# Kernel tuning notes

Measured on AMD Instinct MI355X. Metric: run time of the kernel, lower is better.

## Reference

```python
import jax, jax.numpy as jnp
import numpy as np

TWO_PI = 2.0 * np.pi


def setup_inputs() -> dict:
    key = jax.random.key(0)
    ks = jax.random.split(key, 6)
    n1 = n2 = n3 = 20
    nk, ni, nspin = 4, 16, 2
    # Invertible, physically plausible lattice (~8 Bohr cubic cell + jitter)
    A = jnp.eye(3, dtype=jnp.float32) * 8.0 + 0.05 * jax.random.normal(ks[0], (3, 3), jnp.float32)
    k_grid = 0.1 * jax.random.normal(ks[1], (nk, 3), jnp.float32)
    cg_real = jax.random.normal(ks[2], (nspin, nk, ni, n1, n2, n3), jnp.float32)
    cg_imag = jax.random.normal(ks[3], (nspin, nk, ni, n1, n2, n3), jnp.float32)
    # Real-space evaluation grid: fractional coords in [0,1)^3 mapped through A
    frac = jax.random.uniform(ks[4], (n1, n2, n3, 3), jnp.float32)
    r = frac @ A
    return {"A": A, "k_grid": k_grid, "cg_real": cg_real, "cg_imag": cg_imag, "r": r}


def reference(A, k_grid, cg_real, cg_imag, r):
    # cg: [spin, nk, ni, n1, n2, n3] complex plane-wave coefficients
    cg = cg_real + 1j * cg_imag
    n1, n2, n3 = cg.shape[-3:]
    # Integer FFT frequency mesh m -> reciprocal-lattice vectors G = m @ B,
    # B rows are reciprocal basis: B = 2*pi * inv(A)^T  (A rows = lattice vecs)
    f1 = jnp.fft.fftfreq(n1) * n1
    f2 = jnp.fft.fftfreq(n2) * n2
    f3 = jnp.fft.fftfreq(n3) * n3
    m = jnp.stack(jnp.meshgrid(f1, f2, f3, indexing="ij"), axis=-1).astype(A.dtype)  # [n1,n2,n3,3]
    B = TWO_PI * jnp.linalg.inv(A).T
    G = (m @ B).reshape(-1, 3)                      # [nG, 3]
    vol = jnp.abs(jnp.linalg.det(A))
    Rf = r.reshape(-1, 3)                           # [nR, 3]
    # Plane-wave synthesis: psi_{s,k,i}(r) = exp(i k.r)/sqrt(vol) * sum_G c_G exp(i G.r)
    # (equivalent to the triple-nested vmap over the grid dims, fully vectorized)
    phase_g = jnp.exp(1j * (Rf @ G.T))              # [nR, nG] complex
    dens = cg.reshape(*cg.shape[:3], -1)            # [spin, nk, ni, nG]
    psi = jnp.einsum("skin,rn->skir", dens, phase_g)  # [spin, nk, ni, nR]
    phase_k = jnp.exp(1j * (Rf @ k_grid.T))         # [nR, nk]
    psi = psi * jnp.moveaxis(phase_k, 0, -1)[None, :, None, :]
    psi = psi / jnp.sqrt(vol).astype(psi.real.dtype)
    # [spin, nk, ni, n1, n2, n3] -- matches moveaxis(range(3), range(-3,0))
    return psi.reshape(*cg.shape[:3], *r.shape[:-1])
```

## Files before the change

### kernel.cpp

```cpp
#include <hip/hip_runtime.h>

typedef __attribute__((ext_vector_type(4))) float f32x4;
typedef __attribute__((ext_vector_type(8))) short s16x8;

#define NSKIN 128
#define NG    8000
#define NRPT  8000
#define MT    128
#define NT    128
#define KK    32
#define KCH   1000
#define NKC   8
#define NRB   64
#define TPB   512

__device__ __forceinline__ float sin_rev(float u){ float r; asm("v_sin_f32 %0, %1" : "=v"(r) : "v"(u)); return r; }
__device__ __forceinline__ float cos_rev(float u){ float r; asm("v_cos_f32 %0, %1" : "=v"(r) : "v"(u)); return r; }
__device__ __forceinline__ unsigned int cvt_pk(float lo, float hi){
    unsigned int r; asm("v_cvt_pk_bf16_f32 %0, %1, %2" : "=v"(r) : "v"(lo), "v"(hi)); return r;
}
__device__ __forceinline__ s16x8 bneg(s16x8 v){
    int4 u = *(int4*)&v;
    u.x ^= 0x80008000; u.y ^= 0x80008000; u.z ^= 0x80008000; u.w ^= 0x80008000;
    return *(s16x8*)&u;
}
__device__ __forceinline__ int swz(int row, int kg){
    return row*64 + ((kg ^ ((row>>1)&3))<<4);
}

__global__ __launch_bounds__(TPB, 4) void bloch_mfma4(
    const float* __restrict__ Amat, const float* __restrict__ kgrid,
    const float* __restrict__ cgr,  const float* __restrict__ cgi,
    const float* __restrict__ rpts, float* __restrict__ out, int out_size)
{
    __shared__ float fracS[NT][4];
    __shared__ float rkS[NT][4];
    __shared__ unsigned short Ar[MT*KK], Ai[MT*KK];
    __shared__ unsigned short Bc[NT*KK], Bs[NT*KK];
    __shared__ float invAS[9];
    __shared__ float scaleS;

    const int tid = threadIdx.x;
    const int bid = blockIdx.x;
    const int kc  = bid >> 6;
    const int rb  = bid & 63;
    const int r_base  = rb * NT;
    const int k_begin = kc * KCH;
    const int k_end   = k_begin + KCH;

    if (tid == 0) {
        float a00=Amat[0],a01=Amat[1],a02=Amat[2];
        float a10=Amat[3],a11=Amat[4],a12=Amat[5];
        float a20=Amat[6],a21=Amat[7],a22=Amat[8];
        float c00 =  (a11*a22 - a12*a21);
        float c01 = -(a10*a22 - a12*a20);
        float c02 =  (a10*a21 - a11*a20);
        float det = a00*c00 + a01*c01 + a02*c02;
        float id  = 1.0f/det;
        invAS[0] =  c00*id;
        invAS[1] = -(a01*a22 - a02*a21)*id;
        invAS[2] =  (a01*a12 - a02*a11)*id;
        invAS[3] =  c01*id;
        invAS[4] =  (a00*a22 - a02*a20)*id;
        invAS[5] = -(a00*a12 - a02*a10)*id;
        invAS[6] =  c02*id;
        invAS[7] = -(a00*a21 - a01*a20)*id;
        invAS[8] =  (a00*a11 - a01*a10)*id;
        scaleS   = rsqrtf(fabsf(det));
    }
    __syncthreads();

    if (tid < NT) {
        int rg = r_base + tid; if (rg > NRPT-1) rg = NRPT-1;
        float r0 = rpts[rg*3+0], r1 = rpts[rg*3+1], r2 = rpts[rg*3+2];
        fracS[tid][0] = r0*invAS[0] + r1*invAS[3] + r2*invAS[6];
        fracS[tid][1] = r0*invAS[1] + r1*invAS[4] + r2*invAS[7];
        fracS[tid][2] = r0*invAS[2] + r1*invAS[5] + r2*invAS[8];
        #pragma unroll
        for (int kk = 0; kk < 4; ++kk)
            rkS[tid][kk] = r0*kgrid[kk*3+0] + r1*kgrid[kk*3+1] + r2*kgrid[kk*3+2];
    }
    __syncthreads();

    f32x4 accRe[4][2], accIm[4][2];
    #pragma unroll
    for (int mi = 0; mi < 4; ++mi)
        #pragma unroll
        for (int ni = 0; ni < 2; ++ni) {
            accRe[mi][ni] = (f32x4){0.f,0.f,0.f,0.f};
            accIm[mi][ni] = (f32x4){0.f,0.f,0.f,0.f};
        }

    const int lane = tid & 63;
    const int wid  = tid >> 6;
    const int wm   = wid >> 2;
    const int wn   = wid & 3;
    const int frow = lane & 15;
    const int kq   = lane >> 4;

    const int sa      = tid >> 2;
    const int seg     = tid & 3;
    const int rB      = sa;
    const int quarter = seg;

    const float f0r = fracS[rB][0], f1r = fracS[rB][1], f2r = fracS[rB][2];

    float u1 = f2r - floorf(f2r);
    const float w1c = cos_rev(u1), w1s = sin_rev(u1);
    float yd = -20.0f * f2r; yd -= floorf(yd);
    const float wdc = cos_rev(yd), wds = sin_rev(yd);
    const float w1wdc = w1c*wdc - w1s*wds;
    const float w1wds = w1c*wds + w1s*wdc;

    float4 pvr0, pvr1, pvi0, pvi1;
    {
        int kg = k_begin + seg*8;
        const float* pr_ = &cgr[(size_t)sa*NG + kg];
        const float* pi_ = &cgi[(size_t)sa*NG + kg];
        pvr0 = *(const float4*)pr_;  pvr1 = *(const float4*)(pr_+4);
        pvi0 = *(const float4*)pi_;  pvi1 = *(const float4*)(pi_+4);
    }

    #pragma unroll 1
    for (int kb = k_begin; kb < k_end; kb += KK) {
        __syncthreads();

        {
            uint4 pr, pi;
            pr.x = cvt_pk(pvr0.x, pvr0.y); pr.y = cvt_pk(pvr0.z, pvr0.w);
            pr.z = cvt_pk(pvr1.x, pvr1.y); pr.w = cvt_pk(pvr1.z, pvr1.w);
            pi.x = cvt_pk(pvi0.x, pvi0.y); pi.y = cvt_pk(pvi0.z, pvi0.w);
            pi.z = cvt_pk(pvi1.x, pvi1.y); pi.w = cvt_pk(pvi1.z, pvi1.w);
            *(uint4*)((char*)Ar + swz(sa, seg)) = pr;
            *(uint4*)((char*)Ai + swz(sa, seg)) = pi;
        }
        {
            int g0   = kb + quarter*8;
            int i12  = (g0 * 3277) >> 16;
            int i3_0 = g0 - i12*20;
            int i1a  = (i12 * 3277) >> 16; int i2a = i12 - i1a*20;
            int i12b = i12 + 1;
            int i1b  = (i12b * 3277) >> 16; int i2b = i12b - i1b*20;
            float m1a = (float)(i1a - (i1a >= 10 ? 20 : 0));
            float m2a = (float)(i2a - (i2a >= 10 ? 20 : 0));
            float m1b = (float)(i1b - (i1b >= 10 ? 20 : 0));
            float m2b = (float)(i2b - (i2b >= 10 ? 20 : 0));
            float m30 = (float)(i3_0 - (i3_0 >= 10 ? 20 : 0));
            float y0 = m1a*f0r + m2a*f1r + m30*f2r; y0 -= floorf(y0);
            float cc = cos_rev(y0), cs = sin_rev(y0);
            float rd = (m1b-m1a)*f0r + (m2b-m2a)*f1r; rd -= floorf(rd);
            float rc = cos_rev(rd), rs = sin_rev(rd);
            float wXc = w1c*rc - w1s*rs;
            float wXs = w1c*rs + w1s*rc;
            float bcv[8], bsv[8];
            bcv[0] = cc; bsv[0] = cs;
            #pragma unroll
            for (int j = 1; j < 8; ++j) {
                bool cB = (i3_0 == 20 - j);
                bool cD = (i3_0 == 10 - j);
                float mc = cB ? wXc : (cD ? w1wdc : w1c);
                float ms = cB ? wXs : (cD ? w1wds : w1s);
                float nc = cc*mc - cs*ms;
                float ns = cc*ms + cs*mc;
                cc = nc; cs = ns;
                bcv[j] = cc; bsv[j] = cs;
            }
            uint4 wc, wsn;
            wc.x  = cvt_pk(bcv[0], bcv[1]); wc.y  = cvt_pk(bcv[2], bcv[3]);
            wc.z  = cvt_pk(bcv[4], bcv[5]); wc.w  = cvt_pk(bcv[6], bcv[7]);
            wsn.x = cvt_pk(bsv[0], bsv[1]); wsn.y = cvt_pk(bsv[2], bsv[3]);
            wsn.z = cvt_pk(bsv[4], bsv[5]); wsn.w = cvt_pk(bsv[6], bsv[7]);
            *(uint4*)((char*)Bc + swz(rB, quarter)) = wc;
            *(uint4*)((char*)Bs + swz(rB, quarter)) = wsn;
        }
        {
            int kb2 = kb + KK;
            int kg  = kb2 + seg*8;
            if (kb2 < k_end && kg < k_end) {
                const float* pr_ = &cgr[(size_t)sa*NG + kg];
                const float* pi_ = &cgi[(size_t)sa*NG + kg];
                pvr0 = *(const float4*)pr_;  pvr1 = *(const float4*)(pr_+4);
                pvi0 = *(const float4*)pi_;  pvi1 = *(const float4*)(pi_+4);
            } else {
                pvr0 = make_float4(0.f,0.f,0.f,0.f); pvr1 = pvr0;
                pvi0 = pvr0; pvi1 = pvr0;
            }
        }
        __syncthreads();

        s16x8 bcf[2], bsf[2], bsnf[2];
        #pragma unroll
        for (int ni = 0; ni < 2; ++ni) {
            int col = wn*32 + ni*16 + frow;
            bcf[ni]  = *(const s16x8*)((const char*)Bc + swz(col, kq));
            bsf[ni]  = *(const s16x8*)((const char*)Bs + swz(col, kq));
            bsnf[ni] = bneg(bsf[ni]);
        }
        #pragma unroll
        for (int mi = 0; mi < 4; ++mi) {
            int row = wm*64 + mi*16 + frow;
            s16x8 arf = *(const s16x8*)((const char*)Ar + swz(row, kq));
            s16x8 aif = *(const s16x8*)((const char*)Ai + swz(row, kq));
            #pragma unroll
            for (int ni = 0; ni < 2; ++ni) {
                accRe[mi][ni] = __builtin_amdgcn_mfma_f32_16x16x32_bf16(arf, bcf[ni],  accRe[mi][ni], 0, 0, 0);
                accRe[mi][ni] = __builtin_amdgcn_mfma_f32_16x16x32_bf16(aif, bsnf[ni], accRe[mi][ni], 0, 0, 0);
                accIm[mi][ni] = __builtin_amdgcn_mfma_f32_16x16x32_bf16(arf, bsf[ni],  accIm[mi][ni], 0, 0, 0);
                accIm[mi][ni] = __builtin_amdgcn_mfma_f32_16x16x32_bf16(aif, bcf[ni],  accIm[mi][ni], 0, 0, 0);
            }
        }
    }

    const bool write_imag = (out_size >= 2*NSKIN*NRPT);
    const float scale  = scaleS;
    const float inv2pi = 0.15915494309189535f;
    #pragma unroll
    for (int mi = 0; mi < 4; ++mi) {
        const int m0 = wm*64 + mi*16;
        const int kidx = (m0 >> 4) & 3;
        #pragma unroll
        for (int ni = 0; ni < 2; ++ni) {
            int col = wn*32 + ni*16 + frow;
            int rg = r_base + col;
            if (rg < NRPT) {
                float ang = rkS[col][kidx] * inv2pi;
                float u = ang - floorf(ang);
                float ck = cos_rev(u), sk = sin_rev(u);
                #pragma unroll
                for (int v = 0; v < 4; ++v) {
                    int sg = m0 + (lane >> 4)*4 + v;
                    float re = accRe[mi][ni][v];
                    float im = accIm[mi][ni][v];
                    float orr = (re*ck - im*sk) * scale;
                    size_t lin = (size_t)sg * NRPT + rg;
                    if (write_imag) {
                        float oi = (re*sk + im*ck) * scale;
                        size_t idx = lin * 2;
                        if (idx + 1 < (size_t)out_size) {
                            atomicAdd(&out[idx],   orr);
                            atomicAdd(&out[idx+1], oi);
                        }
                    } else {
                        if (lin < (size_t)out_size)
                            atomicAdd(&out[lin], orr);
                    }
                }
            }
        }
    }
}

extern "C" void kernel_launch(void* const* d_in, const int* in_sizes, int n_in,
                              void* d_out, int out_size, void* d_ws, size_t ws_size,
                              hipStream_t stream) {
    const float* Amat  = (const float*)d_in[0];
    const float* kgrid = (const float*)d_in[1];
    const float* cgr   = (const float*)d_in[2];
    const float* cgi   = (const float*)d_in[3];
    const float* rpts  = (const float*)d_in[4];
    float* out = (float*)d_out;

    hipMemsetAsync(d_out, 0, (size_t)out_size * sizeof(float), stream);

    dim3 grid(NRB * NKC);
    bloch_mfma4<<<grid, TPB, 0, stream>>>(Amat, kgrid, cgr, cgi, rpts, out, out_size);
}
```

Measured before the change: 103.3 us.

## Double-buffer LDS tiles to overlap staging with MFMA and precompute k-phase

Replaces the single shared-memory tile set with two ping-pong buffers, so each iteration reads fragments from one buffer while staging the next tile's coefficients and phase factors into the other. This removes one of the two block barriers per K-step and lets the sin/cos phase generation overlap with the MFMA work. Separately, the per-output exp(ikr) factor is computed once per (r,k) into shared memory instead of being recomputed by every wave. LDS use doubles, which could limit occupancy, and more fragment registers are held live across the staging code.

```diff
diff --git a/kernel.cpp b/kernel.cpp
--- a/kernel.cpp
+++ b/kernel.cpp
@@ -14,6 +14,13 @@
 #define NRB   64
 #define TPB   512
 
+#define TILE_B  8192
+#define BUF_B   (4*TILE_B)
+#define OFF_AR  0
+#define OFF_AI  8192
+#define OFF_BC  16384
+#define OFF_BS  24576
+
 __device__ __forceinline__ float sin_rev(float u){ float r; asm("v_sin_f32 %0, %1" : "=v"(r) : "v"(u)); return r; }
 __device__ __forceinline__ float cos_rev(float u){ float r; asm("v_cos_f32 %0, %1" : "=v"(r) : "v"(u)); return r; }
 __device__ __forceinline__ unsigned int cvt_pk(float lo, float hi){
@@ -28,15 +35,15 @@
     return row*64 + ((kg ^ ((row>>1)&3))<<4);
 }
 
-__global__ __launch_bounds__(TPB, 4) void bloch_mfma4(
+__global__ __launch_bounds__(TPB, 4) void bloch_mfma5(
     const float* __restrict__ Amat, const float* __restrict__ kgrid,
     const float* __restrict__ cgr,  const float* __restrict__ cgi,
     const float* __restrict__ rpts, float* __restrict__ out, int out_size)
 {
+    __shared__ __align__(16) char tiles[2*BUF_B];
     __shared__ float fracS[NT][4];
     __shared__ float rkS[NT][4];
-    __shared__ unsigned short Ar[MT*KK], Ai[MT*KK];
-    __shared__ unsigned short Bc[NT*KK], Bs[NT*KK];
+    __shared__ float2 ekrS[NT][4];
     __shared__ float invAS[9];
     __shared__ float scaleS;
 
@@ -100,10 +107,12 @@
 
     const int sa      = tid >> 2;
     const int seg     = tid & 3;
-    const int rB      = sa;
-    const int quarter = seg;
-
-    const float f0r = fracS[rB][0], f1r = fracS[rB][1], f2r = fracS[rB][2];
+
+    const int stOff = swz(sa, seg);
+    const int aOff  = swz(wm*64 + frow, kq);
+    const int bOff  = swz(wn*32 + frow, kq);
+
+    const float f0r = fracS[sa][0], f1r = fracS[sa][1], f2r = fracS[sa][2];
 
     float u1 = f2r - floorf(f2r);
     const float w1c = cos_rev(u1), w1s = sin_rev(u1);
@@ -113,107 +122,126 @@
     const float w1wds = w1c*wds + w1s*wdc;
 
     float4 pvr0, pvr1, pvi0, pvi1;
-    {
-        int kg = k_begin + seg*8;
-        const float* pr_ = &cgr[(size_t)sa*NG + kg];
-        const float* pi_ = &cgi[(size_t)sa*NG + kg];
-        pvr0 = *(const float4*)pr_;  pvr1 = *(const float4*)(pr_+4);
-        pvi0 = *(const float4*)pi_;  pvi1 = *(const float4*)(pi_+4);
-    }
-
+
+    auto loadA = [&](int kb){
+        int kg = kb + seg*8;
+        if (kb < k_end && kg < k_end) {
+            const float* pr_ = &cgr[(size_t)sa*NG + kg];
+            const float* pi_ = &cgi[(size_t)sa*NG + kg];
+            pvr0 = *(const float4*)pr_;  pvr1 = *(const float4*)(pr_+4);
+            pvi0 = *(const float4*)pi_;  pvi1 = *(const float4*)(pi_+4);
+        } else {
+            pvr0 = make_float4(0.f,0.f,0.f,0.f); pvr1 = pvr0;
+            pvi0 = pvr0; pvi1 = pvr0;
+        }
+    };
+    auto stageA = [&](char* wb){
+        uint4 pr, pi;
+        pr.x = cvt_pk(pvr0.x, pvr0.y); pr.y = cvt_pk(pvr0.z, pvr0.w);
+        pr.z = cvt_pk(pvr1.x, pvr1.y); pr.w = cvt_pk(pvr1.z, pvr1.w);
+        pi.x = cvt_pk(pvi0.x, pvi0.y); pi.y = cvt_pk(pvi0.z, pvi0.w);
+        pi.z = cvt_pk(pvi1.x, pvi1.y); pi.w = cvt_pk(pvi1.z, pvi1.w);
+        *(uint4*)(wb + OFF_AR + stOff) = pr;
+        *(uint4*)(wb + OFF_AI + stOff) = pi;
+    };
+    auto stageB = [&](int kb, char* wb){
+        int g0   = kb + seg*8;
+        int i12  = (g0 * 3277) >> 16;
+        int i3_0 = g0 - i12*20;
+        int i1a  = (i12 * 3277) >> 16; int i2a = i12 - i1a*20;
+        int i12b = i12 + 1;
+        int i1b  = (i12b * 3277) >> 16; int i2b = i12b - i1b*20;
+        float m1a = (float)(i1a - (i1a >= 10 ? 20 : 0));
+        float m2a = (float)(i2a - (i2a >= 10 ? 20 : 0));
+        float m1b = (float)(i1b - (i1b >= 10 ? 20 : 0));
+        float m2b = (float)(i2b - (i2b >= 10 ? 20 : 0));
+        float m30 = (float)(i3_0 - (i3_0 >= 10 ? 20 : 0));
+        float y0 = m1a*f0r + m2a*f1r + m30*f2r; y0 -= floorf(y0);
+        float cc = cos_rev(y0), cs = sin_rev(y0);
+        float rd = (m1b-m1a)*f0r + (m2b-m2a)*f1r; rd -= floorf(rd);
+        float rc = cos_rev(rd), rs = sin_rev(rd);
+        float wXc = w1c*rc - w1s*rs;
+        float wXs = w1c*rs + w1s*rc;
+        float bcv[8], bsv[8];
+        bcv[0] = cc; bsv[0] = cs;
+        #pragma unroll
+        for (int j = 1; j < 8; ++j) {
+            bool cB = (i3_0 == 20 - j);
+            bool cD = (i3_0 == 10 - j);
+            float mc = cB ? wXc : (cD ? w1wdc : w1c);
+            float ms = cB ? wXs : (cD ? w1wds : w1s);
+            float nc = cc*mc - cs*ms;
+            float ns = cc*ms + cs*mc;
+            cc = nc; cs = ns;
+            bcv[j] = cc; bsv[j] = cs;
+        }
+        uint4 wc, wsn;
+        wc.x  = cvt_pk(bcv[0], bcv[1]); wc.y  = cvt_pk(bcv[2], bcv[3]);
+        wc.z  = cvt_pk(bcv[4], bcv[5]); wc.w  = cvt_pk(bcv[6], bcv[7]);
+        wsn.x = cvt_pk(bsv[0], bsv[1]); wsn.y = cvt_pk(bsv[2], bsv[3]);
+        wsn.z = cvt_pk(bsv[4], bsv[5]); wsn.w = cvt_pk(bsv[6], bsv[7]);
+        *(uint4*)(wb + OFF_BC + stOff) = wc;
+        *(uint4*)(wb + OFF_BS + stOff) = wsn;
+    };
+
+    loadA(k_begin);
+    stageA(tiles);
+    stageB(k_begin, tiles);
+    loadA(k_begin + KK);
+    __syncthreads();
+
+    int p = 0;
     #pragma unroll 1
     for (int kb = k_begin; kb < k_end; kb += KK) {
-        __syncthreads();
-
-        {
-            uint4 pr, pi;
-            pr.x = cvt_pk(pvr0.x, pvr0.y); pr.y = cvt_pk(pvr0.z, pvr0.w);
-            pr.z = cvt_pk(pvr1.x, pvr1.y); pr.w = cvt_pk(pvr1.z, pvr1.w);
-            pi.x = cvt_pk(pvi0.x, pvi0.y); pi.y = cvt_pk(pvi0.z, pvi0.w);
-            pi.z = cvt_pk(pvi1.x, pvi1.y); pi.w = cvt_pk(pvi1.z, pvi1.w);
-            *(uint4*)((char*)Ar + swz(sa, seg)) = pr;
-            *(uint4*)((char*)Ai + swz(sa, seg)) = pi;
-        }
-        {
-            int g0   = kb + quarter*8;
-            int i12  = (g0 * 3277) >> 16;
-            int i3_0 = g0 - i12*20;
-            int i1a  = (i12 * 3277) >> 16; int i2a = i12 - i1a*20;
-            int i12b = i12 + 1;
-            int i1b  = (i12b * 3277) >> 16; int i2b = i12b - i1b*20;
-            float m1a = (float)(i1a - (i1a >= 10 ? 20 : 0));
-            float m2a = (float)(i2a - (i2a >= 10 ? 20 : 0));
-            float m1b = (float)(i1b - (i1b >= 10 ? 20 : 0));
-            float m2b = (float)(i2b - (i2b >= 10 ? 20 : 0));
-            float m30 = (float)(i3_0 - (i3_0 >= 10 ? 20 : 0));
-            float y0 = m1a*f0r + m2a*f1r + m30*f2r; y0 -= floorf(y0);
-            float cc = cos_rev(y0), cs = sin_rev(y0);
-            float rd = (m1b-m1a)*f0r + (m2b-m2a)*f1r; rd -= floorf(rd);
-            float rc = cos_rev(rd), rs = sin_rev(rd);
-            float wXc = w1c*rc - w1s*rs;
-            float wXs = w1c*rs + w1s*rc;
-            float bcv[8], bsv[8];
-            bcv[0] = cc; bsv[0] = cs;
-            #pragma unroll
-            for (int j = 1; j < 8; ++j) {
-                bool cB = (i3_0 == 20 - j);
-                bool cD = (i3_0 == 10 - j);
-                float mc = cB ? wXc : (cD ? w1wdc : w1c);
-                float ms = cB ? wXs : (cD ? w1wds : w1s);
-                float nc = cc*mc - cs*ms;
-                float ns = cc*ms + cs*mc;
-                cc = nc; cs = ns;
-                bcv[j] = cc; bsv[j] = cs;
-            }
-            uint4 wc, wsn;
-            wc.x  = cvt_pk(bcv[0], bcv[1]); wc.y  = cvt_pk(bcv[2], bcv[3]);
-            wc.z  = cvt_pk(bcv[4], bcv[5]); wc.w  = cvt_pk(bcv[6], bcv[7]);
-            wsn.x = cvt_pk(bsv[0], bsv[1]); wsn.y = cvt_pk(bsv[2], bsv[3]);
-            wsn.z = cvt_pk(bsv[4], bsv[5]); wsn.w = cvt_pk(bsv[6], bsv[7]);
-            *(uint4*)((char*)Bc + swz(rB, quarter)) = wc;
-            *(uint4*)((char*)Bs + swz(rB, quarter)) = wsn;
-        }
-        {
-            int kb2 = kb + KK;
-            int kg  = kb2 + seg*8;
-            if (kb2 < k_end && kg < k_end) {
-                const float* pr_ = &cgr[(size_t)sa*NG + kg];
-                const float* pi_ = &cgi[(size_t)sa*NG + kg];
-                pvr0 = *(const float4*)pr_;  pvr1 = *(const float4*)(pr_+4);
-                pvi0 = *(const float4*)pi_;  pvi1 = *(const float4*)(pi_+4);
-            } else {
-                pvr0 = make_float4(0.f,0.f,0.f,0.f); pvr1 = pvr0;
-                pvi0 = pvr0; pvi1 = pvr0;
-            }
-        }
-        __syncthreads();
+        const char* rb_ = tiles + p*BUF_B;
+        char*       wb_ = tiles + (p^1)*BUF_B;
+        const bool hn = (kb + KK < k_end);
 
         s16x8 bcf[2], bsf[2], bsnf[2];
         #pragma unroll
         for (int ni = 0; ni < 2; ++ni) {
-            int col = wn*32 + ni*16 + frow;
-            bcf[ni]  = *(const s16x8*)((const char*)Bc + swz(col, kq));
-            bsf[ni]  = *(const s16x8*)((const char*)Bs + swz(col, kq));
+            bcf[ni]  = *(const s16x8*)(rb_ + OFF_BC + bOff + ni*1024);
+            bsf[ni]  = *(const s16x8*)(rb_ + OFF_BS + bOff + ni*1024);
             bsnf[ni] = bneg(bsf[ni]);
         }
+        s16x8 arf[4], aif[4];
         #pragma unroll
         for (int mi = 0; mi < 4; ++mi) {
-            int row = wm*64 + mi*16 + frow;
-            s16x8 arf = *(const s16x8*)((const char*)Ar + swz(row, kq));
-            s16x8 aif = *(const s16x8*)((const char*)Ai + swz(row, kq));
+            arf[mi] = *(const s16x8*)(rb_ + OFF_AR + aOff + mi*1024);
+            aif[mi] = *(const s16x8*)(rb_ + OFF_AI + aOff + mi*1024);
+        }
+
+        if (hn) {
+            stageA(wb_);
+            stageB(kb + KK, wb_);
+            loadA(kb + 2*KK);
+        }
+
+        #pragma unroll
+        for (int mi = 0; mi < 4; ++mi)
             #pragma unroll
             for (int ni = 0; ni < 2; ++ni) {
-                accRe[mi][ni] = __builtin_amdgcn_mfma_f32_16x16x32_bf16(arf, bcf[ni],  accRe[mi][ni], 0, 0, 0);
-                accRe[mi][ni] = __builtin_amdgcn_mfma_f32_16x16x32_bf16(aif, bsnf[ni], accRe[mi][ni], 0, 0, 0);
-                accIm[mi][ni] = __builtin_amdgcn_mfma_f32_16x16x32_bf16(arf, bsf[ni],  accIm[mi][ni], 0, 0, 0);
-                accIm[mi][ni] = __builtin_amdgcn_mfma_f32_16x16x32_bf16(aif, bcf[ni],  accIm[mi][ni], 0, 0, 0);
+                accRe[mi][ni] = __builtin_amdgcn_mfma_f32_16x16x32_bf16(arf[mi], bcf[ni],  accRe[mi][ni], 0, 0, 0);
+                accRe[mi][ni] = __builtin_amdgcn_mfma_f32_16x16x32_bf16(aif[mi], bsnf[ni], accRe[mi][ni], 0, 0, 0);
+                accIm[mi][ni] = __builtin_amdgcn_mfma_f32_16x16x32_bf16(arf[mi], bsf[ni],  accIm[mi][ni], 0, 0, 0);
+                accIm[mi][ni] = __builtin_amdgcn_mfma_f32_16x16x32_bf16(aif[mi], bcf[ni],  accIm[mi][ni], 0, 0, 0);
             }
-        }
-    }
+
+        __syncthreads();
+        p ^= 1;
+    }
+
+    {
+        int col = tid >> 2, kidx = tid & 3;
+        const float inv2pi = 0.15915494309189535f;
+        float ang = rkS[col][kidx] * inv2pi;
+        float u = ang - floorf(ang);
+        ekrS[col][kidx] = make_float2(cos_rev(u), sin_rev(u));
+    }
+    __syncthreads();
 
     const bool write_imag = (out_size >= 2*NSKIN*NRPT);
-    const float scale  = scaleS;
-    const float inv2pi = 0.15915494309189535f;
+    const float scale = scaleS;
     #pragma unroll
     for (int mi = 0; mi < 4; ++mi) {
         const int m0 = wm*64 + mi*16;
@@ -223,12 +251,11 @@
             int col = wn*32 + ni*16 + frow;
             int rg = r_base + col;
             if (rg < NRPT) {
-                float ang = rkS[col][kidx] * inv2pi;
-                float u = ang - floorf(ang);
-                float ck = cos_rev(u), sk = sin_rev(u);
+                float2 ekr = ekrS[col][kidx];
+                float ck = ekr.x, sk = ekr.y;
                 #pragma unroll
                 for (int v = 0; v < 4; ++v) {
-                    int sg = m0 + (lane >> 4)*4 + v;
+                    int sg = m0 + kq*4 + v;
                     float re = accRe[mi][ni][v];
                     float im = accIm[mi][ni][v];
                     float orr = (re*ck - im*sk) * scale;
@@ -263,5 +290,5 @@
     hipMemsetAsync(d_out, 0, (size_t)out_size * sizeof(float), stream);
 
     dim3 grid(NRB * NKC);
-    bloch_mfma4<<<grid, TPB, 0, stream>>>(Amat, kgrid, cgr, cgi, rpts, out, out_size);
-}
+    bloch_mfma5<<<grid, TPB, 0, stream>>>(Amat, kgrid, cgr, cgi, rpts, out, out_size);
+}
```

Measured after the change: 199.9 us. 93.5% more time.

## Pre-convert coefficients to swizzled bf16 tiles and load them directly into LDS

Applied to the files above, without the earlier changes.

Adds a prepass kernel that converts the complex coefficients to bf16 and stores them in a workspace, already swizzled to the LDS layout. The main kernel then streams those tiles into shared memory with global_load_lds and no longer converts in registers. Tiles shrink to 128x64 with 256 threads, and the k-chunking changes to 10 chunks of 800 so the work divides evenly. The Bloch k-phase factors are now computed once into shared memory after the main loop. The cost is an extra launch and workspace traffic, and the register-prefetch overlap of the old loop is dropped.

```diff
diff --git a/kernel.cpp b/kernel.cpp
--- a/kernel.cpp
+++ b/kernel.cpp
@@ -3,16 +3,25 @@
 typedef __attribute__((ext_vector_type(4))) float f32x4;
 typedef __attribute__((ext_vector_type(8))) short s16x8;
 
-#define NSKIN 128
-#define NG    8000
-#define NRPT  8000
-#define MT    128
-#define NT    128
-#define KK    32
-#define KCH   1000
-#define NKC   8
-#define NRB   64
-#define TPB   512
+#define NG     8000
+#define NRPT   8000
+#define NSKIN  128
+#define MT     128
+#define NT     64
+#define KK     32
+#define KCH    800
+#define NKC    10
+#define NTILES 25
+#define NRB    125
+#define TPB    256
+#define WS_TILE_B 16384
+#define WS_NEED   ((size_t)NKC*NTILES*WS_TILE_B)
+
+#define S_AR 0
+#define S_AI 8192
+#define S_BC 16384
+#define S_BS 20480
+#define S_SZ 24576
 
 __device__ __forceinline__ float sin_rev(float u){ float r; asm("v_sin_f32 %0, %1" : "=v"(r) : "v"(u)); return r; }
 __device__ __forceinline__ float cos_rev(float u){ float r; asm("v_cos_f32 %0, %1" : "=v"(r) : "v"(u)); return r; }
@@ -27,26 +36,54 @@
 __device__ __forceinline__ int swz(int row, int kg){
     return row*64 + ((kg ^ ((row>>1)&3))<<4);
 }
-
-__global__ __launch_bounds__(TPB, 4) void bloch_mfma4(
+__device__ __forceinline__ void glds16(const void* g, void* l){
+    __builtin_amdgcn_global_load_lds((const __attribute__((address_space(1))) void*)g,
+                                     (__attribute__((address_space(3))) void*)l, 16, 0, 0);
+}
+
+__global__ __launch_bounds__(256) void bloch_prepass(
+    const float* __restrict__ cgr, const float* __restrict__ cgi,
+    char* __restrict__ ws)
+{
+    int gid = blockIdx.x*256 + threadIdx.x;
+    if (gid >= NKC*NTILES*2*512) return;
+    int slot  = gid & 3;
+    int row   = (gid >> 2) & 127;
+    int pt    = gid >> 9;
+    int plane = pt & 1;
+    int tileIdx = pt >> 1;
+    int t  = tileIdx % NTILES;
+    int kc = tileIdx / NTILES;
+    int kg = slot ^ ((row >> 1) & 3);
+    int k  = kc*KCH + t*KK + kg*8;
+    const float* src = plane ? cgi : cgr;
+    const float4 v0 = *(const float4*)&src[(size_t)row*NG + k];
+    const float4 v1 = *(const float4*)&src[(size_t)row*NG + k + 4];
+    uint4 p;
+    p.x = cvt_pk(v0.x, v0.y); p.y = cvt_pk(v0.z, v0.w);
+    p.z = cvt_pk(v1.x, v1.y); p.w = cvt_pk(v1.z, v1.w);
+    *(uint4*)(ws + (size_t)gid*16) = p;
+}
+
+template<bool PRE>
+__global__ __launch_bounds__(TPB, 6) void bloch7(
     const float* __restrict__ Amat, const float* __restrict__ kgrid,
     const float* __restrict__ cgr,  const float* __restrict__ cgi,
-    const float* __restrict__ rpts, float* __restrict__ out, int out_size)
+    const float* __restrict__ rpts, const char* __restrict__ ws,
+    float* __restrict__ out, int out_size)
 {
+    __shared__ __align__(16) char smem[S_SZ];
     __shared__ float fracS[NT][4];
-    __shared__ float rkS[NT][4];
-    __shared__ unsigned short Ar[MT*KK], Ai[MT*KK];
-    __shared__ unsigned short Bc[NT*KK], Bs[NT*KK];
     __shared__ float invAS[9];
     __shared__ float scaleS;
 
     const int tid = threadIdx.x;
     const int bid = blockIdx.x;
-    const int kc  = bid >> 6;
-    const int rb  = bid & 63;
+    const int kc  = bid >> 7;
+    const int rb  = bid & 127;
+    if (rb >= NRB) return;
     const int r_base  = rb * NT;
     const int k_begin = kc * KCH;
-    const int k_end   = k_begin + KCH;
 
     if (tid == 0) {
         float a00=Amat[0],a01=Amat[1],a02=Amat[2];
@@ -71,14 +108,11 @@
     __syncthreads();
 
     if (tid < NT) {
-        int rg = r_base + tid; if (rg > NRPT-1) rg = NRPT-1;
+        int rg = r_base + tid;
         float r0 = rpts[rg*3+0], r1 = rpts[rg*3+1], r2 = rpts[rg*3+2];
         fracS[tid][0] = r0*invAS[0] + r1*invAS[3] + r2*invAS[6];
         fracS[tid][1] = r0*invAS[1] + r1*invAS[4] + r2*invAS[7];
         fracS[tid][2] = r0*invAS[2] + r1*invAS[5] + r2*invAS[8];
-        #pragma unroll
-        for (int kk = 0; kk < 4; ++kk)
-            rkS[tid][kk] = r0*kgrid[kk*3+0] + r1*kgrid[kk*3+1] + r2*kgrid[kk*3+2];
     }
     __syncthreads();
 
@@ -93,17 +127,18 @@
 
     const int lane = tid & 63;
     const int wid  = tid >> 6;
-    const int wm   = wid >> 2;
-    const int wn   = wid & 3;
+    const int wm   = wid >> 1;
+    const int wn   = wid & 1;
     const int frow = lane & 15;
     const int kq   = lane >> 4;
 
-    const int sa      = tid >> 2;
-    const int seg     = tid & 3;
-    const int rB      = sa;
-    const int quarter = seg;
-
-    const float f0r = fracS[rB][0], f1r = fracS[rB][1], f2r = fracS[rB][2];
+    const int sB   = tid >> 2;
+    const int qtr  = tid & 3;
+    const int stOffB = swz(sB, qtr);
+    const int aOff   = swz(wm*64 + frow, kq);
+    const int bOff   = swz(wn*32 + frow, kq);
+
+    const float f0r = fracS[sB][0], f1r = fracS[sB][1], f2r = fracS[sB][2];
 
     float u1 = f2r - floorf(f2r);
     const float w1c = cos_rev(u1), w1s = sin_rev(u1);
@@ -112,30 +147,38 @@
     const float w1wdc = w1c*wdc - w1s*wds;
     const float w1wds = w1c*wds + w1s*wdc;
 
-    float4 pvr0, pvr1, pvi0, pvi1;
-    {
-        int kg = k_begin + seg*8;
-        const float* pr_ = &cgr[(size_t)sa*NG + kg];
-        const float* pi_ = &cgi[(size_t)sa*NG + kg];
-        pvr0 = *(const float4*)pr_;  pvr1 = *(const float4*)(pr_+4);
-        pvi0 = *(const float4*)pi_;  pvi1 = *(const float4*)(pi_+4);
-    }
-
     #pragma unroll 1
-    for (int kb = k_begin; kb < k_end; kb += KK) {
-        __syncthreads();
+    for (int t = 0; t < NTILES; ++t) {
+        const int kb = k_begin + t*KK;
+
+        if (PRE) {
+            const char* tb = ws + (size_t)(kc*NTILES + t)*WS_TILE_B;
+            glds16(tb +         tid*16,        smem + S_AR +        tid*16);
+            glds16(tb + 4096 +  tid*16,        smem + S_AR + 4096 + tid*16);
+            glds16(tb + 8192 +  tid*16,        smem + S_AI +        tid*16);
+            glds16(tb + 12288 + tid*16,        smem + S_AI + 4096 + tid*16);
+        } else {
+            #pragma unroll
+            for (int j = 0; j < 2; ++j) {
+                int row = (tid>>2) + 64*j;
+                int kg  = qtr ^ ((row>>1)&3);
+                int k   = kb + kg*8;
+                const float4 v0r = *(const float4*)&cgr[(size_t)row*NG + k];
+                const float4 v1r = *(const float4*)&cgr[(size_t)row*NG + k + 4];
+                const float4 v0i = *(const float4*)&cgi[(size_t)row*NG + k];
+                const float4 v1i = *(const float4*)&cgi[(size_t)row*NG + k + 4];
+                uint4 pr, pi;
+                pr.x = cvt_pk(v0r.x, v0r.y); pr.y = cvt_pk(v0r.z, v0r.w);
+                pr.z = cvt_pk(v1r.x, v1r.y); pr.w = cvt_pk(v1r.z, v1r.w);
+                pi.x = cvt_pk(v0i.x, v0i.y); pi.y = cvt_pk(v0i.z, v0i.w);
+                pi.z = cvt_pk(v1i.x, v1i.y); pi.w = cvt_pk(v1i.z, v1i.w);
+                *(uint4*)(smem + S_AR + row*64 + qtr*16) = pr;
+                *(uint4*)(smem + S_AI + row*64 + qtr*16) = pi;
+            }
+        }
 
         {
-            uint4 pr, pi;
-            pr.x = cvt_pk(pvr0.x, pvr0.y); pr.y = cvt_pk(pvr0.z, pvr0.w);
-            pr.z = cvt_pk(pvr1.x, pvr1.y); pr.w = cvt_pk(pvr1.z, pvr1.w);
-            pi.x = cvt_pk(pvi0.x, pvi0.y); pi.y = cvt_pk(pvi0.z, pvi0.w);
-            pi.z = cvt_pk(pvi1.x, pvi1.y); pi.w = cvt_pk(pvi1.z, pvi1.w);
-            *(uint4*)((char*)Ar + swz(sa, seg)) = pr;
-            *(uint4*)((char*)Ai + swz(sa, seg)) = pi;
-        }
-        {
-            int g0   = kb + quarter*8;
+            int g0   = kb + qtr*8;
             int i12  = (g0 * 3277) >> 16;
             int i3_0 = g0 - i12*20;
             int i1a  = (i12 * 3277) >> 16; int i2a = i12 - i1a*20;
@@ -170,37 +213,22 @@
             wc.z  = cvt_pk(bcv[4], bcv[5]); wc.w  = cvt_pk(bcv[6], bcv[7]);
             wsn.x = cvt_pk(bsv[0], bsv[1]); wsn.y = cvt_pk(bsv[2], bsv[3]);
             wsn.z = cvt_pk(bsv[4], bsv[5]); wsn.w = cvt_pk(bsv[6], bsv[7]);
-            *(uint4*)((char*)Bc + swz(rB, quarter)) = wc;
-            *(uint4*)((char*)Bs + swz(rB, quarter)) = wsn;
-        }
-        {
-            int kb2 = kb + KK;
-            int kg  = kb2 + seg*8;
-            if (kb2 < k_end && kg < k_end) {
-                const float* pr_ = &cgr[(size_t)sa*NG + kg];
-                const float* pi_ = &cgi[(size_t)sa*NG + kg];
-                pvr0 = *(const float4*)pr_;  pvr1 = *(const float4*)(pr_+4);
-                pvi0 = *(const float4*)pi_;  pvi1 = *(const float4*)(pi_+4);
-            } else {
-                pvr0 = make_float4(0.f,0.f,0.f,0.f); pvr1 = pvr0;
-                pvi0 = pvr0; pvi1 = pvr0;
-            }
+            *(uint4*)(smem + S_BC + stOffB) = wc;
+            *(uint4*)(smem + S_BS + stOffB) = wsn;
         }
         __syncthreads();
 
         s16x8 bcf[2], bsf[2], bsnf[2];
         #pragma unroll
         for (int ni = 0; ni < 2; ++ni) {
-            int col = wn*32 + ni*16 + frow;
-            bcf[ni]  = *(const s16x8*)((const char*)Bc + swz(col, kq));
-            bsf[ni]  = *(const s16x8*)((const char*)Bs + swz(col, kq));
+            bcf[ni]  = *(const s16x8*)(smem + S_BC + bOff + ni*1024);
+            bsf[ni]  = *(const s16x8*)(smem + S_BS + bOff + ni*1024);
             bsnf[ni] = bneg(bsf[ni]);
         }
         #pragma unroll
         for (int mi = 0; mi < 4; ++mi) {
-            int row = wm*64 + mi*16 + frow;
-            s16x8 arf = *(const s16x8*)((const char*)Ar + swz(row, kq));
-            s16x8 aif = *(const s16x8*)((const char*)Ai + swz(row, kq));
+            s16x8 arf = *(const s16x8*)(smem + S_AR + aOff + mi*1024);
+            s16x8 aif = *(const s16x8*)(smem + S_AI + aOff + mi*1024);
             #pragma unroll
             for (int ni = 0; ni < 2; ++ni) {
                 accRe[mi][ni] = __builtin_amdgcn_mfma_f32_16x16x32_bf16(arf, bcf[ni],  accRe[mi][ni], 0, 0, 0);
@@ -209,11 +237,23 @@
                 accIm[mi][ni] = __builtin_amdgcn_mfma_f32_16x16x32_bf16(aif, bcf[ni],  accIm[mi][ni], 0, 0, 0);
             }
         }
-    }
+        __syncthreads();
+    }
+
+    float2* ekr = (float2*)smem;
+    {
+        int col = tid >> 2, kidx = tid & 3;
+        int rg = r_base + col;
+        float r0 = rpts[rg*3+0], r1 = rpts[rg*3+1], r2 = rpts[rg*3+2];
+        float ang = (r0*kgrid[kidx*3+0] + r1*kgrid[kidx*3+1] + r2*kgrid[kidx*3+2])
+                    * 0.15915494309189535f;
+        float u = ang - floorf(ang);
+        ekr[col*4+kidx] = make_float2(cos_rev(u), sin_rev(u));
+    }
+    __syncthreads();
 
     const bool write_imag = (out_size >= 2*NSKIN*NRPT);
-    const float scale  = scaleS;
-    const float inv2pi = 0.15915494309189535f;
+    const float scale = scaleS;
     #pragma unroll
     for (int mi = 0; mi < 4; ++mi) {
         const int m0 = wm*64 + mi*16;
@@ -222,28 +262,24 @@
         for (int ni = 0; ni < 2; ++ni) {
             int col = wn*32 + ni*16 + frow;
             int rg = r_base + col;
-            if (rg < NRPT) {
-                float ang = rkS[col][kidx] * inv2pi;
-                float u = ang - floorf(ang);
-                float ck = cos_rev(u), sk = sin_rev(u);
-                #pragma unroll
-                for (int v = 0; v < 4; ++v) {
-                    int sg = m0 + (lane >> 4)*4 + v;
-                    float re = accRe[mi][ni][v];
-                    float im = accIm[mi][ni][v];
-                    float orr = (re*ck - im*sk) * scale;
-                    size_t lin = (size_t)sg * NRPT + rg;
-                    if (write_imag) {
-                        float oi = (re*sk + im*ck) * scale;
-                        size_t idx = lin * 2;
-                        if (idx + 1 < (size_t)out_size) {
-                            atomicAdd(&out[idx],   orr);
-                            atomicAdd(&out[idx+1], oi);
-                        }
-                    } else {
-                        if (lin < (size_t)out_size)
-                            atomicAdd(&out[lin], orr);
+            float2 e = ekr[col*4+kidx];
+            float ck = e.x, sk = e.y;
+            #pragma unroll
+            for (int v = 0; v < 4; ++v) {
+                int sg = m0 + kq*4 + v;
+                float re = accRe[mi][ni][v];
+                float im = accIm[mi][ni][v];
+                float orr = (re*ck - im*sk) * scale;
+                size_t lin = (size_t)sg * NRPT + rg;
+                if (write_imag) {
+                    float oi = (re*sk + im*ck) * scale;
+                    size_t idx = lin * 2;
+                    if (idx + 1 < (size_t)out_size) {
+                        atomicAdd(&out[idx],   orr);
+                        atomicAdd(&out[idx+1], oi);
                     }
+                } else {
+                    atomicAdd(&out[lin], orr);
                 }
             }
         }
@@ -262,6 +298,14 @@
 
     hipMemsetAsync(d_out, 0, (size_t)out_size * sizeof(float), stream);
 
-    dim3 grid(NRB * NKC);
-    bloch_mfma4<<<grid, TPB, 0, stream>>>(Amat, kgrid, cgr, cgi, rpts, out, out_size);
-}
+    const bool use_pre = (ws_size >= WS_NEED);
+    dim3 grid(NKC * 128);
+    if (use_pre) {
+        bloch_prepass<<<dim3(NKC*NTILES*2*512/256), 256, 0, stream>>>(cgr, cgi, (char*)d_ws);
+        bloch7<true><<<grid, TPB, 0, stream>>>(Amat, kgrid, cgr, cgi, rpts,
+                                               (const char*)d_ws, out, out_size);
+    } else {
+        bloch7<false><<<grid, TPB, 0, stream>>>(Amat, kgrid, cgr, cgi, rpts,
+                                                nullptr, out, out_size);
+    }
+}
```

Result: slower. 339.9 us (+228.9%).
